# Kernel optimization log

Hardware: AMD Instinct MI355X
Metric: run time of the kernel (lower is better)

Reference implementation:

```python
import jax, jax.numpy as jnp
import numpy as np

EPS = 1e-5


def _gcn_conv(h, W, b, src, dst, norm, N):
    # h: (B, N, F_in) -> linear transform then normalized neighbor aggregation
    h = h @ W                                  # (B, N, H)
    msg = h[:, src, :] * norm[None, :, None]   # gather + edge norm, (B, E, H)
    agg = jax.vmap(lambda m: jax.ops.segment_sum(m, dst, num_segments=N))(msg)
    return agg + b


def _batchnorm(h, gamma, beta):
    # BatchNorm1d over flattened (B*N, H), training-mode batch statistics
    B, N, H = h.shape
    f = h.reshape(-1, H)
    mean = f.mean(axis=0)
    var = f.var(axis=0)
    f = (f - mean) * jax.lax.rsqrt(var + EPS) * gamma + beta
    return f.reshape(B, N, H)


def setup_inputs() -> dict:
    key = jax.random.key(0)
    ks = jax.random.split(key, 6)
    B, N, E, IN, H, OUT = 2, 20000, 640000, 128, 128, 10
    x = jax.random.normal(ks[0], (B, N, IN), dtype=jnp.float32)
    edge_index = jax.random.randint(ks[1], (2, E), 0, N, dtype=jnp.int64)
    W1 = jax.random.normal(ks[2], (IN, H), dtype=jnp.float32) / np.sqrt(IN)
    W2 = jax.random.normal(ks[3], (H, H), dtype=jnp.float32) / np.sqrt(H)
    Wc = jax.random.normal(ks[4], (H, OUT), dtype=jnp.float32) / np.sqrt(H)
    return {
        "x": x,
        "W1": W1, "b1": jnp.zeros((H,), jnp.float32),
        "W2": W2, "b2": jnp.zeros((H,), jnp.float32),
        "g1": jnp.ones((H,), jnp.float32), "bt1": jnp.zeros((H,), jnp.float32),
        "g2": jnp.ones((H,), jnp.float32), "bt2": jnp.zeros((H,), jnp.float32),
        "Wc": Wc, "bc": jnp.zeros((OUT,), jnp.float32),
        "edge_index": edge_index,
    }


def reference(x, W1, b1, W2, b2, g1, bt1, g2, bt2, Wc, bc, edge_index):
    N = x.shape[1]
    loops = jnp.arange(N, dtype=edge_index.dtype)
    src = jnp.concatenate([edge_index[0], loops])  # add self-loops (GCNConv default)
    dst = jnp.concatenate([edge_index[1], loops])
    deg = jax.ops.segment_sum(jnp.ones(src.shape[0], x.dtype), dst, num_segments=N)
    dinv = jnp.where(deg > 0, jax.lax.rsqrt(deg), 0.0)
    norm = dinv[src] * dinv[dst]                   # symmetric GCN normalization

    h = jax.nn.relu(_gcn_conv(x, W1, b1, src, dst, norm, N))
    h = _batchnorm(h, g1, bt1)
    # dropout is identity in eval mode
    h = jax.nn.relu(_gcn_conv(h, W2, b2, src, dst, norm, N))
    h = _batchnorm(h, g2, bt2)
    return h @ Wc + bc                              # (B, N, out_dim)
```

## Files before the change

### kernel.cpp

```cpp
#include <hip/hip_runtime.h>
#include <hip/hip_bf16.h>


constexpr int Nn   = 20000;
constexpr int Ee   = 640000;
constexpr int OUTd = 10;
constexpr int Mm   = 2 * Nn;
constexpr int ELLW = 96;
constexpr int NSLOT = 64;
#define EPSV 1e-5f
constexpr float INV_M = 1.0f / (float)Mm;

using frag16 = __attribute__((ext_vector_type(8))) short;
using f32x4  = __attribute__((ext_vector_type(4))) float;

__device__ inline short bf(float f) {
    union { __hip_bfloat16 h; short s; } u;
    u.h = __float2bfloat16(f);
    return u.s;
}
__device__ inline float lo16(unsigned u) { union { unsigned v; float f; } x; x.v = u << 16;        return x.f; }
__device__ inline float hi16(unsigned u) { union { unsigned v; float f; } x; x.v = u & 0xffff0000u; return x.f; }
__device__ inline unsigned pack2(float f0, float f1) {
    return (unsigned)(unsigned short)bf(f0) | ((unsigned)(unsigned short)bf(f1) << 16);
}

__global__ __launch_bounds__(256) void scatter_ell_k(const int* __restrict__ src, const int* __restrict__ dst,
                                                     int* __restrict__ cnt, int* __restrict__ ell) {
    int e = blockIdx.x * 256 + threadIdx.x;
    if (e < Ee) {
        int d = dst[e];
        int pos = atomicAdd(&cnt[d], 1);
        if (pos < ELLW) ell[(size_t)d * ELLW + pos] = src[e];
    }
}

__global__ __launch_bounds__(256) void dinv_k(const int* __restrict__ cnt, float* __restrict__ dinv) {
    int n = blockIdx.x * 256 + threadIdx.x;
    if (n < Nn) dinv[n] = rsqrtf((float)cnt[n] + 1.0f);
}

__global__ __launch_bounds__(256) void gemm1_k(const float* __restrict__ A,
                                               const float* __restrict__ W,
                                               const float* __restrict__ dinv,
                                               unsigned short* __restrict__ Hout) {
    __shared__ short Wl[128 * 136];
    int t = threadIdx.x;

    for (int it = 0; it < 8; ++it) {
        int lin = it * 256 + t;
        int kp  = lin & 63;
        int n4  = (lin >> 6) * 4;
        float4 w0 = *(const float4*)(W + (size_t)(2 * kp) * 128 + n4);
        float4 w1 = *(const float4*)(W + (size_t)(2 * kp + 1) * 128 + n4);
        *(unsigned*)&Wl[(n4 + 0) * 136 + 2 * kp] = pack2(w0.x, w1.x);
        *(unsigned*)&Wl[(n4 + 1) * 136 + 2 * kp] = pack2(w0.y, w1.y);
        *(unsigned*)&Wl[(n4 + 2) * 136 + 2 * kp] = pack2(w0.z, w1.z);
        *(unsigned*)&Wl[(n4 + 3) * 136 + 2 * kp] = pack2(w0.w, w1.w);
    }
    __syncthreads();

    int wv = t >> 6, l = t & 63;
    int row_q = l >> 4, lane16 = l & 15;
    int row0 = blockIdx.x * 64 + wv * 16;

    frag16 a[4];
    const float* Arow = A + (size_t)(row0 + lane16) * 128;
    #pragma unroll
    for (int q = 0; q < 4; ++q) {
        int k0 = q * 32 + row_q * 8;
        float4 v0 = *(const float4*)(Arow + k0);
        float4 v1 = *(const float4*)(Arow + k0 + 4);
        frag16 fa = { bf(v0.x), bf(v0.y), bf(v0.z), bf(v0.w),
                      bf(v1.x), bf(v1.y), bf(v1.z), bf(v1.w) };
        a[q] = fa;
    }

    f32x4 acc[8];
    #pragma unroll
    for (int c = 0; c < 8; ++c) acc[c] = (f32x4){0.f, 0.f, 0.f, 0.f};

    #pragma unroll
    for (int c = 0; c < 8; ++c) {
        int n = c * 16 + lane16;
        #pragma unroll
        for (int q = 0; q < 4; ++q) {
            int k0 = q * 32 + row_q * 8;
            frag16 b = *(const frag16*)&Wl[n * 136 + k0];
            acc[c] = __builtin_amdgcn_mfma_f32_16x16x32_bf16(a[q], b, acc[c], 0, 0, 0);
        }
    }

    #pragma unroll
    for (int r = 0; r < 4; ++r) {
        int rg = row0 + row_q * 4 + r;
        int b  = rg >= Nn;
        int n  = rg - b * Nn;
        float dv = dinv[n];
        unsigned short* dst = Hout + (size_t)n * 256 + b * 128;
        #pragma unroll
        for (int c = 0; c < 8; ++c)
            dst[c * 16 + lane16] = (unsigned short)bf(acc[c][r] * dv);
    }
}

__global__ __launch_bounds__(256) void gemm2_k(const unsigned short* __restrict__ Abf,
                                               const float* __restrict__ W,
                                               const float* __restrict__ g,
                                               const float* __restrict__ bt,
                                               const float* __restrict__ S,
                                               const float* __restrict__ dinv,
                                               unsigned short* __restrict__ Hout) {
    __shared__ short Wl[128 * 136];
    __shared__ float al[128], cl[128], dpart[2][128];
    int t = threadIdx.x;

    if (t < 128) {
        float s = 0.f, ss = 0.f;
        #pragma unroll 8
        for (int k = 0; k < NSLOT; ++k) {
            s  += S[k * 256 + t];
            ss += S[k * 256 + 128 + t];
        }
        float m   = s * INV_M;
        float var = ss * INV_M - m * m;
        float a   = g[t] * rsqrtf(var + EPSV);
        float c   = bt[t] - m * a;
        al[t] = a; cl[t] = c;
    }
    __syncthreads();

    for (int it = 0; it < 8; ++it) {
        int lin = it * 256 + t;
        int kp  = lin & 63;
        int n4  = (lin >> 6) * 4;
        float a0 = al[2 * kp], a1 = al[2 * kp + 1];
        float4 w0 = *(const float4*)(W + (size_t)(2 * kp) * 128 + n4);
        float4 w1 = *(const float4*)(W + (size_t)(2 * kp + 1) * 128 + n4);
        w0.x *= a0; w0.y *= a0; w0.z *= a0; w0.w *= a0;
        w1.x *= a1; w1.y *= a1; w1.z *= a1; w1.w *= a1;
        *(unsigned*)&Wl[(n4 + 0) * 136 + 2 * kp] = pack2(w0.x, w1.x);
        *(unsigned*)&Wl[(n4 + 1) * 136 + 2 * kp] = pack2(w0.y, w1.y);
        *(unsigned*)&Wl[(n4 + 2) * 136 + 2 * kp] = pack2(w0.z, w1.z);
        *(unsigned*)&Wl[(n4 + 3) * 136 + 2 * kp] = pack2(w0.w, w1.w);
    }

    {
        int col = t & 127, hh = t >> 7;
        const float* Wc0 = W + (size_t)(hh * 64) * 128 + col;
        float dp = 0.f;
        #pragma unroll 8
        for (int k = 0; k < 64; ++k) dp += cl[hh * 64 + k] * Wc0[(size_t)k * 128];
        dpart[hh][col] = dp;
    }
    __syncthreads();

    int wv = t >> 6, l = t & 63;
    int row_q = l >> 4, lane16 = l & 15;
    int row0 = blockIdx.x * 64 + wv * 16;

    int rgA = row0 + lane16;
    int bA  = rgA >= Nn;
    int nA  = rgA - bA * Nn;
    const unsigned short* Arow = Abf + (size_t)nA * 256 + bA * 128;
    frag16 a[4];
    #pragma unroll
    for (int q = 0; q < 4; ++q) {
        int k0 = q * 32 + row_q * 8;
        a[q] = *(const frag16*)(Arow + k0);
    }

    f32x4 acc[8];
    #pragma unroll
    for (int c = 0; c < 8; ++c) {
        int n = c * 16 + lane16;
        float d = dpart[0][n] + dpart[1][n];
        acc[c] = (f32x4){d, d, d, d};
    }

    #pragma unroll
    for (int c = 0; c < 8; ++c) {
        int n = c * 16 + lane16;
        #pragma unroll
        for (int q = 0; q < 4; ++q) {
            int k0 = q * 32 + row_q * 8;
            frag16 b = *(const frag16*)&Wl[n * 136 + k0];
            acc[c] = __builtin_amdgcn_mfma_f32_16x16x32_bf16(a[q], b, acc[c], 0, 0, 0);
        }
    }

    #pragma unroll
    for (int r = 0; r < 4; ++r) {
        int rg = row0 + row_q * 4 + r;
        int b  = rg >= Nn;
        int n  = rg - b * Nn;
        float dv = dinv[n];
        unsigned short* dst = Hout + (size_t)n * 256 + b * 128;
        #pragma unroll
        for (int c = 0; c < 8; ++c)
            dst[c * 16 + lane16] = (unsigned short)bf(acc[c][r] * dv);
    }
}

__device__ inline void acc8(const uint4& v, float& a0, float& a1, float& a2, float& a3,
                            float& a4, float& a5, float& a6, float& a7) {
    a0 += lo16(v.x); a1 += hi16(v.x);
    a2 += lo16(v.y); a3 += hi16(v.y);
    a4 += lo16(v.z); a5 += hi16(v.z);
    a6 += lo16(v.w); a7 += hi16(v.w);
}

__global__ __launch_bounds__(256) void agg_k(const unsigned short* __restrict__ h,
                                             const int* __restrict__ ell,
                                             const int* __restrict__ cnt,
                                             const float* __restrict__ dinv,
                                             const float* __restrict__ bias,
                                             unsigned short* __restrict__ act,
                                             float* __restrict__ S) {
    int t  = threadIdx.x;
    int wv = t >> 6;
    int l  = t & 63;
    int n  = __builtin_amdgcn_readfirstlane(blockIdx.x * 4 + wv);
    int half = l >> 5;
    int g    = l & 31;

    const uint4* h4 = (const uint4*)h;

    float a0 = 0.f, a1 = 0.f, a2 = 0.f, a3 = 0.f, a4 = 0.f, a5 = 0.f, a6 = 0.f, a7 = 0.f;

    int deg = cnt[n]; if (deg > ELLW) deg = ELLW;
    const int* row = ell + (size_t)n * ELLW;

    int j = 0;
    for (; j + 15 < deg; j += 16) {
        int i0 = row[j +  0 + half], i1 = row[j +  2 + half];
        int i2 = row[j +  4 + half], i3 = row[j +  6 + half];
        int i4 = row[j +  8 + half], i5 = row[j + 10 + half];
        int i6 = row[j + 12 + half], i7 = row[j + 14 + half];
        uint4 v0 = h4[(size_t)i0 * 32 + g];
        uint4 v1 = h4[(size_t)i1 * 32 + g];
        uint4 v2 = h4[(size_t)i2 * 32 + g];
        uint4 v3 = h4[(size_t)i3 * 32 + g];
        uint4 v4 = h4[(size_t)i4 * 32 + g];
        uint4 v5 = h4[(size_t)i5 * 32 + g];
        uint4 v6 = h4[(size_t)i6 * 32 + g];
        uint4 v7 = h4[(size_t)i7 * 32 + g];
        acc8(v0, a0, a1, a2, a3, a4, a5, a6, a7);
        acc8(v1, a0, a1, a2, a3, a4, a5, a6, a7);
        acc8(v2, a0, a1, a2, a3, a4, a5, a6, a7);
        acc8(v3, a0, a1, a2, a3, a4, a5, a6, a7);
        acc8(v4, a0, a1, a2, a3, a4, a5, a6, a7);
        acc8(v5, a0, a1, a2, a3, a4, a5, a6, a7);
        acc8(v6, a0, a1, a2, a3, a4, a5, a6, a7);
        acc8(v7, a0, a1, a2, a3, a4, a5, a6, a7);
    }
    for (; j + 3 < deg; j += 4) {
        int i0 = row[j + half];
        int i1 = row[j + 2 + half];
        uint4 v0 = h4[(size_t)i0 * 32 + g];
        uint4 v1 = h4[(size_t)i1 * 32 + g];
        acc8(v0, a0, a1, a2, a3, a4, a5, a6, a7);
        acc8(v1, a0, a1, a2, a3, a4, a5, a6, a7);
    }
    for (; j + 1 < deg; j += 2) {
        int i0 = row[j + half];
        uint4 v0 = h4[(size_t)i0 * 32 + g];
        acc8(v0, a0, a1, a2, a3, a4, a5, a6, a7);
    }
    if (j < deg) {
        if (half == 0) {
            int i0 = row[j];
            uint4 v0 = h4[(size_t)i0 * 32 + g];
            acc8(v0, a0, a1, a2, a3, a4, a5, a6, a7);
        }
    }

    a0 += __shfl_xor(a0, 32); a1 += __shfl_xor(a1, 32);
    a2 += __shfl_xor(a2, 32); a3 += __shfl_xor(a3, 32);
    a4 += __shfl_xor(a4, 32); a5 += __shfl_xor(a5, 32);
    a6 += __shfl_xor(a6, 32); a7 += __shfl_xor(a7, 32);

    float dn = dinv[n];
    uint4 u  = h4[(size_t)n * 32 + g];
    int cb   = (g & 15) * 8;
    float4 b0 = *(const float4*)(bias + cb);
    float4 b1 = *(const float4*)(bias + cb + 4);
    float o0 = fmaxf(fmaf(dn, a0 + lo16(u.x), b0.x), 0.f);
    float o1 = fmaxf(fmaf(dn, a1 + hi16(u.x), b0.y), 0.f);
    float o2 = fmaxf(fmaf(dn, a2 + lo16(u.y), b0.z), 0.f);
    float o3 = fmaxf(fmaf(dn, a3 + hi16(u.y), b0.w), 0.f);
    float o4 = fmaxf(fmaf(dn, a4 + lo16(u.z), b1.x), 0.f);
    float o5 = fmaxf(fmaf(dn, a5 + hi16(u.z), b1.y), 0.f);
    float o6 = fmaxf(fmaf(dn, a6 + lo16(u.w), b1.z), 0.f);
    float o7 = fmaxf(fmaf(dn, a7 + hi16(u.w), b1.w), 0.f);

    if (l < 32) {
        uint4 st;
        st.x = pack2(o0, o1); st.y = pack2(o2, o3);
        st.z = pack2(o4, o5); st.w = pack2(o6, o7);
        *(uint4*)(act + (size_t)n * 256 + (size_t)g * 8) = st;
    }

    float q0 = o0 * o0, q1 = o1 * o1, q2 = o2 * o2, q3 = o3 * o3;
    float q4 = o4 * o4, q5 = o5 * o5, q6 = o6 * o6, q7 = o7 * o7;
    float s0 = o0 + __shfl_xor(o0, 16), s1 = o1 + __shfl_xor(o1, 16);
    float s2 = o2 + __shfl_xor(o2, 16), s3 = o3 + __shfl_xor(o3, 16);
    float s4 = o4 + __shfl_xor(o4, 16), s5 = o5 + __shfl_xor(o5, 16);
    float s6 = o6 + __shfl_xor(o6, 16), s7 = o7 + __shfl_xor(o7, 16);
    float t0 = q0 + __shfl_xor(q0, 16), t1 = q1 + __shfl_xor(q1, 16);
    float t2 = q2 + __shfl_xor(q2, 16), t3 = q3 + __shfl_xor(q3, 16);
    float t4 = q4 + __shfl_xor(q4, 16), t5 = q5 + __shfl_xor(q5, 16);
    float t6 = q6 + __shfl_xor(q6, 16), t7 = q7 + __shfl_xor(q7, 16);

    __shared__ float sh[4][16][17];
    if (l < 16) {
        float* p = sh[wv][l];
        p[0] = s0; p[1] = s1; p[2] = s2; p[3] = s3;
        p[4] = s4; p[5] = s5; p[6] = s6; p[7] = s7;
        p[8]  = t0; p[9]  = t1; p[10] = t2; p[11] = t3;
        p[12] = t4; p[13] = t5; p[14] = t6; p[15] = t7;
    }
    __syncthreads();
    int col  = t & 127, stat = t >> 7;
    int gi   = col >> 3, slot = (col & 7) + stat * 8;
    float v = sh[0][gi][slot] + sh[1][gi][slot] + sh[2][gi][slot] + sh[3][gi][slot];
    atomicAdd(&S[(blockIdx.x & (NSLOT - 1)) * 256 + stat * 128 + col], v);
}

__global__ __launch_bounds__(256) void gemmout_k(const unsigned short* __restrict__ act,
                                                 const float* __restrict__ Wc,
                                                 const float* __restrict__ bc,
                                                 const float* __restrict__ g,
                                                 const float* __restrict__ bt,
                                                 const float* __restrict__ S,
                                                 float* __restrict__ out) {
    __shared__ float Wl[128 * OUTd];
    __shared__ float bl[OUTd];
    __shared__ float al[128], cl[128];
    int t = threadIdx.x;
    for (int i = t; i < 128 * OUTd; i += 256) Wl[i] = Wc[i];
    if (t < OUTd) bl[t] = bc[t];
    if (t < 128) {
        float s = 0.f, ss = 0.f;
        #pragma unroll 8
        for (int k = 0; k < NSLOT; ++k) {
            s  += S[k * 256 + t];
            ss += S[k * 256 + 128 + t];
        }
        float m   = s * INV_M;
        float var = ss * INV_M - m * m;
        float a   = g[t] * rsqrtf(var + EPSV);
        al[t] = a;
        cl[t] = bt[t] - m * a;
    }
    __syncthreads();

    int r = blockIdx.x * 256 + t;
    if (r >= Mm) return;
    int b = r >= Nn;
    int n = r - b * Nn;

    float acc[OUTd];
    #pragma unroll
    for (int jj = 0; jj < OUTd; jj++) acc[jj] = 0.f;

    const uint4* a4 = (const uint4*)(act + (size_t)n * 256 + b * 128);
    #pragma unroll 4
    for (int k4 = 0; k4 < 16; k4++) {
        uint4 u = a4[k4];
        int k = k4 * 8;
        float e0 = lo16(u.x) * al[k+0] + cl[k+0];
        float e1 = hi16(u.x) * al[k+1] + cl[k+1];
        float e2 = lo16(u.y) * al[k+2] + cl[k+2];
        float e3 = hi16(u.y) * al[k+3] + cl[k+3];
        float e4 = lo16(u.z) * al[k+4] + cl[k+4];
        float e5 = hi16(u.z) * al[k+5] + cl[k+5];
        float e6 = lo16(u.w) * al[k+6] + cl[k+6];
        float e7 = hi16(u.w) * al[k+7] + cl[k+7];
        #pragma unroll
        for (int jj = 0; jj < OUTd; jj++) {
            acc[jj] += e0 * Wl[(k+0) * OUTd + jj];
            acc[jj] += e1 * Wl[(k+1) * OUTd + jj];
            acc[jj] += e2 * Wl[(k+2) * OUTd + jj];
            acc[jj] += e3 * Wl[(k+3) * OUTd + jj];
            acc[jj] += e4 * Wl[(k+4) * OUTd + jj];
            acc[jj] += e5 * Wl[(k+5) * OUTd + jj];
            acc[jj] += e6 * Wl[(k+6) * OUTd + jj];
            acc[jj] += e7 * Wl[(k+7) * OUTd + jj];
        }
    }
    #pragma unroll
    for (int jj = 0; jj < OUTd; jj++) out[(size_t)r * OUTd + jj] = acc[jj] + bl[jj];
}

extern "C" void kernel_launch(void* const* d_in, const int* in_sizes, int n_in,
                              void* d_out, int out_size, void* d_ws, size_t ws_size,
                              hipStream_t stream) {
    (void)in_sizes; (void)n_in; (void)out_size; (void)ws_size;

    const float* x   = (const float*)d_in[0];
    const float* W1  = (const float*)d_in[1];
    const float* b1  = (const float*)d_in[2];
    const float* W2  = (const float*)d_in[3];
    const float* b2  = (const float*)d_in[4];
    const float* g1  = (const float*)d_in[5];
    const float* bt1 = (const float*)d_in[6];
    const float* g2  = (const float*)d_in[7];
    const float* bt2 = (const float*)d_in[8];
    const float* Wc  = (const float*)d_in[9];
    const float* bc  = (const float*)d_in[10];
    const int*   ei  = (const int*)d_in[11];
    const int* srcp = ei;
    const int* dstp = ei + Ee;

    char* ws = (char*)d_ws;
    size_t off = 0;
    auto alloc = [&](size_t bytes) -> void* {
        void* p = ws + off;
        off += (bytes + 511) & ~(size_t)511;
        return p;
    };
    unsigned short* h   = (unsigned short*)alloc((size_t)Mm * 128 * 2);
    unsigned short* act = (unsigned short*)alloc((size_t)Mm * 128 * 2);
    float* dinv = (float*)alloc(Nn * 4);
    int*   cnt  = (int*)alloc(Nn * 4 + 2 * NSLOT * 256 * 4);
    float* S1   = (float*)(cnt + Nn);
    float* S2   = S1 + NSLOT * 256;
    int*   ell  = (int*)alloc((size_t)Nn * ELLW * 4);

    float* out = (float*)d_out;

    hipMemsetAsync(cnt, 0, Nn * 4 + 2 * NSLOT * 256 * 4, stream);
    scatter_ell_k<<<(Ee + 255) / 256, 256, 0, stream>>>(srcp, dstp, cnt, ell);
    dinv_k<<<(Nn + 255) / 256, 256, 0, stream>>>(cnt, dinv);

    gemm1_k<<<Mm / 64, 256, 0, stream>>>(x, W1, dinv, h);
    agg_k<<<Nn / 4, 256, 0, stream>>>(h, ell, cnt, dinv, b1, act, S1);

    gemm2_k<<<Mm / 64, 256, 0, stream>>>(act, W2, g1, bt1, S1, dinv, h);
    agg_k<<<Nn / 4, 256, 0, stream>>>(h, ell, cnt, dinv, b2, act, S2);

    gemmout_k<<<(Mm + 255) / 256, 256, 0, stream>>>(act, Wc, bc, g2, bt2, S2, out);
}
```

Before: 244.6 us.

## Fuse edge scatter with first GEMM and compute degree norms inside aggregation

```diff
diff --git a/kernel.cpp b/kernel.cpp
--- a/kernel.cpp
+++ b/kernel.cpp
@@ -8,6 +8,8 @@
 constexpr int Mm   = 2 * Nn;
 constexpr int ELLW = 96;
 constexpr int NSLOT = 64;
+constexpr int SCB  = (Ee + 255) / 256;
+constexpr int GMB  = Mm / 64;
 #define EPSV 1e-5f
 constexpr float INV_M = 1.0f / (float)Mm;
 
@@ -25,27 +27,25 @@
     return (unsigned)(unsigned short)bf(f0) | ((unsigned)(unsigned short)bf(f1) << 16);
 }
 
-__global__ __launch_bounds__(256) void scatter_ell_k(const int* __restrict__ src, const int* __restrict__ dst,
-                                                     int* __restrict__ cnt, int* __restrict__ ell) {
-    int e = blockIdx.x * 256 + threadIdx.x;
-    if (e < Ee) {
-        int d = dst[e];
-        int pos = atomicAdd(&cnt[d], 1);
-        if (pos < ELLW) ell[(size_t)d * ELLW + pos] = src[e];
-    }
-}
-
-__global__ __launch_bounds__(256) void dinv_k(const int* __restrict__ cnt, float* __restrict__ dinv) {
-    int n = blockIdx.x * 256 + threadIdx.x;
-    if (n < Nn) dinv[n] = rsqrtf((float)cnt[n] + 1.0f);
-}
-
-__global__ __launch_bounds__(256) void gemm1_k(const float* __restrict__ A,
-                                               const float* __restrict__ W,
-                                               const float* __restrict__ dinv,
-                                               unsigned short* __restrict__ Hout) {
+__global__ __launch_bounds__(256) void fg1_k(const int* __restrict__ src, const int* __restrict__ dst,
+                                             int* __restrict__ cnt, int* __restrict__ ell,
+                                             const float* __restrict__ A,
+                                             const float* __restrict__ W,
+                                             unsigned short* __restrict__ Hout) {
     __shared__ short Wl[128 * 136];
     int t = threadIdx.x;
+
+    if (blockIdx.x < SCB) {
+        int e = blockIdx.x * 256 + t;
+        if (e < Ee) {
+            int d = dst[e];
+            int pos = atomicAdd(&cnt[d], 1);
+            if (pos < ELLW) ell[(size_t)d * ELLW + pos] = src[e];
+        }
+        return;
+    }
+
+    int bid = blockIdx.x - SCB;
 
     for (int it = 0; it < 8; ++it) {
         int lin = it * 256 + t;
@@ -62,7 +62,7 @@
 
     int wv = t >> 6, l = t & 63;
     int row_q = l >> 4, lane16 = l & 15;
-    int row0 = blockIdx.x * 64 + wv * 16;
+    int row0 = bid * 64 + wv * 16;
 
     frag16 a[4];
     const float* Arow = A + (size_t)(row0 + lane16) * 128;
@@ -96,11 +96,10 @@
         int rg = row0 + row_q * 4 + r;
         int b  = rg >= Nn;
         int n  = rg - b * Nn;
-        float dv = dinv[n];
-        unsigned short* dst = Hout + (size_t)n * 256 + b * 128;
+        unsigned short* dstp = Hout + (size_t)n * 256 + b * 128;
         #pragma unroll
         for (int c = 0; c < 8; ++c)
-            dst[c * 16 + lane16] = (unsigned short)bf(acc[c][r] * dv);
+            dstp[c * 16 + lane16] = (unsigned short)bf(acc[c][r]);
     }
 }
 
@@ -109,7 +108,6 @@
                                                const float* __restrict__ g,
                                                const float* __restrict__ bt,
                                                const float* __restrict__ S,
-                                               const float* __restrict__ dinv,
                                                unsigned short* __restrict__ Hout) {
     __shared__ short Wl[128 * 136];
     __shared__ float al[128], cl[128], dpart[2][128];
@@ -194,26 +192,26 @@
         int rg = row0 + row_q * 4 + r;
         int b  = rg >= Nn;
         int n  = rg - b * Nn;
-        float dv = dinv[n];
         unsigned short* dst = Hout + (size_t)n * 256 + b * 128;
         #pragma unroll
         for (int c = 0; c < 8; ++c)
-            dst[c * 16 + lane16] = (unsigned short)bf(acc[c][r] * dv);
-    }
-}
-
-__device__ inline void acc8(const uint4& v, float& a0, float& a1, float& a2, float& a3,
+            dst[c * 16 + lane16] = (unsigned short)bf(acc[c][r]);
+    }
+}
+
+__device__ inline void accw(const uint4& v, float w,
+                            float& a0, float& a1, float& a2, float& a3,
                             float& a4, float& a5, float& a6, float& a7) {
-    a0 += lo16(v.x); a1 += hi16(v.x);
-    a2 += lo16(v.y); a3 += hi16(v.y);
-    a4 += lo16(v.z); a5 += hi16(v.z);
-    a6 += lo16(v.w); a7 += hi16(v.w);
-}
+    a0 = fmaf(w, lo16(v.x), a0); a1 = fmaf(w, hi16(v.x), a1);
+    a2 = fmaf(w, lo16(v.y), a2); a3 = fmaf(w, hi16(v.y), a3);
+    a4 = fmaf(w, lo16(v.z), a4); a5 = fmaf(w, hi16(v.z), a5);
+    a6 = fmaf(w, lo16(v.w), a6); a7 = fmaf(w, hi16(v.w), a7);
+}
+__device__ inline float wdeg(int c) { return rsqrtf((float)c + 1.0f); }
 
 __global__ __launch_bounds__(256) void agg_k(const unsigned short* __restrict__ h,
                                              const int* __restrict__ ell,
                                              const int* __restrict__ cnt,
-                                             const float* __restrict__ dinv,
                                              const float* __restrict__ bias,
                                              unsigned short* __restrict__ act,
                                              float* __restrict__ S) {
@@ -228,8 +226,12 @@
 
     float a0 = 0.f, a1 = 0.f, a2 = 0.f, a3 = 0.f, a4 = 0.f, a5 = 0.f, a6 = 0.f, a7 = 0.f;
 
-    int deg = cnt[n]; if (deg > ELLW) deg = ELLW;
+    int degc = cnt[n];
+    float dn = wdeg(degc);
+    int deg = degc > ELLW ? ELLW : degc;
     const int* row = ell + (size_t)n * ELLW;
+
+    uint4 u = h4[(size_t)n * 32 + g];
 
     int j = 0;
     for (; j + 15 < deg; j += 16) {
@@ -237,6 +239,8 @@
         int i2 = row[j +  4 + half], i3 = row[j +  6 + half];
         int i4 = row[j +  8 + half], i5 = row[j + 10 + half];
         int i6 = row[j + 12 + half], i7 = row[j + 14 + half];
+        int c0 = cnt[i0], c1 = cnt[i1], c2 = cnt[i2], c3 = cnt[i3];
+        int c4 = cnt[i4], c5 = cnt[i5], c6 = cnt[i6], c7 = cnt[i7];
         uint4 v0 = h4[(size_t)i0 * 32 + g];
         uint4 v1 = h4[(size_t)i1 * 32 + g];
         uint4 v2 = h4[(size_t)i2 * 32 + g];
@@ -245,33 +249,36 @@
         uint4 v5 = h4[(size_t)i5 * 32 + g];
         uint4 v6 = h4[(size_t)i6 * 32 + g];
         uint4 v7 = h4[(size_t)i7 * 32 + g];
-        acc8(v0, a0, a1, a2, a3, a4, a5, a6, a7);
-        acc8(v1, a0, a1, a2, a3, a4, a5, a6, a7);
-        acc8(v2, a0, a1, a2, a3, a4, a5, a6, a7);
-        acc8(v3, a0, a1, a2, a3, a4, a5, a6, a7);
-        acc8(v4, a0, a1, a2, a3, a4, a5, a6, a7);
-        acc8(v5, a0, a1, a2, a3, a4, a5, a6, a7);
-        acc8(v6, a0, a1, a2, a3, a4, a5, a6, a7);
-        acc8(v7, a0, a1, a2, a3, a4, a5, a6, a7);
+        accw(v0, wdeg(c0), a0, a1, a2, a3, a4, a5, a6, a7);
+        accw(v1, wdeg(c1), a0, a1, a2, a3, a4, a5, a6, a7);
+        accw(v2, wdeg(c2), a0, a1, a2, a3, a4, a5, a6, a7);
+        accw(v3, wdeg(c3), a0, a1, a2, a3, a4, a5, a6, a7);
+        accw(v4, wdeg(c4), a0, a1, a2, a3, a4, a5, a6, a7);
+        accw(v5, wdeg(c5), a0, a1, a2, a3, a4, a5, a6, a7);
+        accw(v6, wdeg(c6), a0, a1, a2, a3, a4, a5, a6, a7);
+        accw(v7, wdeg(c7), a0, a1, a2, a3, a4, a5, a6, a7);
     }
     for (; j + 3 < deg; j += 4) {
         int i0 = row[j + half];
         int i1 = row[j + 2 + half];
+        int c0 = cnt[i0], c1 = cnt[i1];
         uint4 v0 = h4[(size_t)i0 * 32 + g];
         uint4 v1 = h4[(size_t)i1 * 32 + g];
-        acc8(v0, a0, a1, a2, a3, a4, a5, a6, a7);
-        acc8(v1, a0, a1, a2, a3, a4, a5, a6, a7);
+        accw(v0, wdeg(c0), a0, a1, a2, a3, a4, a5, a6, a7);
+        accw(v1, wdeg(c1), a0, a1, a2, a3, a4, a5, a6, a7);
     }
     for (; j + 1 < deg; j += 2) {
         int i0 = row[j + half];
+        int c0 = cnt[i0];
         uint4 v0 = h4[(size_t)i0 * 32 + g];
-        acc8(v0, a0, a1, a2, a3, a4, a5, a6, a7);
+        accw(v0, wdeg(c0), a0, a1, a2, a3, a4, a5, a6, a7);
     }
     if (j < deg) {
         if (half == 0) {
             int i0 = row[j];
+            int c0 = cnt[i0];
             uint4 v0 = h4[(size_t)i0 * 32 + g];
-            acc8(v0, a0, a1, a2, a3, a4, a5, a6, a7);
+            accw(v0, wdeg(c0), a0, a1, a2, a3, a4, a5, a6, a7);
         }
     }
 
@@ -280,19 +287,21 @@
     a4 += __shfl_xor(a4, 32); a5 += __shfl_xor(a5, 32);
     a6 += __shfl_xor(a6, 32); a7 += __shfl_xor(a7, 32);
 
-    float dn = dinv[n];
-    uint4 u  = h4[(size_t)n * 32 + g];
     int cb   = (g & 15) * 8;
     float4 b0 = *(const float4*)(bias + cb);
     float4 b1 = *(const float4*)(bias + cb + 4);
-    float o0 = fmaxf(fmaf(dn, a0 + lo16(u.x), b0.x), 0.f);
-    float o1 = fmaxf(fmaf(dn, a1 + hi16(u.x), b0.y), 0.f);
-    float o2 = fmaxf(fmaf(dn, a2 + lo16(u.y), b0.z), 0.f);
-    float o3 = fmaxf(fmaf(dn, a3 + hi16(u.y), b0.w), 0.f);
-    float o4 = fmaxf(fmaf(dn, a4 + lo16(u.z), b1.x), 0.f);
-    float o5 = fmaxf(fmaf(dn, a5 + hi16(u.z), b1.y), 0.f);
-    float o6 = fmaxf(fmaf(dn, a6 + lo16(u.w), b1.z), 0.f);
-    float o7 = fmaxf(fmaf(dn, a7 + hi16(u.w), b1.w), 0.f);
+    float i0v = fmaf(dn, lo16(u.x), a0), i1v = fmaf(dn, hi16(u.x), a1);
+    float i2v = fmaf(dn, lo16(u.y), a2), i3v = fmaf(dn, hi16(u.y), a3);
+    float i4v = fmaf(dn, lo16(u.z), a4), i5v = fmaf(dn, hi16(u.z), a5);
+    float i6v = fmaf(dn, lo16(u.w), a6), i7v = fmaf(dn, hi16(u.w), a7);
+    float o0 = fmaxf(fmaf(dn, i0v, b0.x), 0.f);
+    float o1 = fmaxf(fmaf(dn, i1v, b0.y), 0.f);
+    float o2 = fmaxf(fmaf(dn, i2v, b0.z), 0.f);
+    float o3 = fmaxf(fmaf(dn, i3v, b0.w), 0.f);
+    float o4 = fmaxf(fmaf(dn, i4v, b1.x), 0.f);
+    float o5 = fmaxf(fmaf(dn, i5v, b1.y), 0.f);
+    float o6 = fmaxf(fmaf(dn, i6v, b1.z), 0.f);
+    float o7 = fmaxf(fmaf(dn, i7v, b1.w), 0.f);
 
     if (l < 32) {
         uint4 st;
@@ -422,7 +431,6 @@
     };
     unsigned short* h   = (unsigned short*)alloc((size_t)Mm * 128 * 2);
     unsigned short* act = (unsigned short*)alloc((size_t)Mm * 128 * 2);
-    float* dinv = (float*)alloc(Nn * 4);
     int*   cnt  = (int*)alloc(Nn * 4 + 2 * NSLOT * 256 * 4);
     float* S1   = (float*)(cnt + Nn);
     float* S2   = S1 + NSLOT * 256;
@@ -431,14 +439,12 @@
     float* out = (float*)d_out;
 
     hipMemsetAsync(cnt, 0, Nn * 4 + 2 * NSLOT * 256 * 4, stream);
-    scatter_ell_k<<<(Ee + 255) / 256, 256, 0, stream>>>(srcp, dstp, cnt, ell);
-    dinv_k<<<(Nn + 255) / 256, 256, 0, stream>>>(cnt, dinv);
-
-    gemm1_k<<<Mm / 64, 256, 0, stream>>>(x, W1, dinv, h);
-    agg_k<<<Nn / 4, 256, 0, stream>>>(h, ell, cnt, dinv, b1, act, S1);
-
-    gemm2_k<<<Mm / 64, 256, 0, stream>>>(act, W2, g1, bt1, S1, dinv, h);
-    agg_k<<<Nn / 4, 256, 0, stream>>>(h, ell, cnt, dinv, b2, act, S2);
+    fg1_k<<<SCB + GMB, 256, 0, stream>>>(srcp, dstp, cnt, ell, x, W1, h);
+
+    agg_k<<<Nn / 4, 256, 0, stream>>>(h, ell, cnt, b1, act, S1);
+
+    gemm2_k<<<Mm / 64, 256, 0, stream>>>(act, W2, g1, bt1, S1, h);
+    agg_k<<<Nn / 4, 256, 0, stream>>>(h, ell, cnt, b2, act, S2);
 
     gemmout_k<<<(Mm + 255) / 256, 256, 0, stream>>>(act, Wc, bc, g2, bt2, S2, out);
 }
```

New measurement: 245.4 us. No clear change (+0.3%).
